# Kernel optimization log

Measured on AMD Instinct MI355X. Metric: run time of the kernel, lower is better.

Reference implementation:

```python
import jax, jax.numpy as jnp
import numpy as np

B, T, D_IN, H, LAT = 256, 512, 32, 128, 64


def lstm_scan(x, Wih, Whh, bih, bhh):
    """PyTorch-convention single-layer LSTM over x [B,T,D] -> hidden states [B,T,H].
    Gate order: i, f, g, o. Gates = x@Wih.T + bih + h@Whh.T + bhh."""
    Bm, _, _ = x.shape
    Hm = Whh.shape[1]
    # precompute input contributions for all timesteps: [B,T,4H]
    xg = jnp.einsum('btd,gd->btg', x, Wih) + bih + bhh

    def step(carry, g_t):
        h, c = carry
        gates = g_t + h @ Whh.T  # [B,4H]
        i, f, g, o = jnp.split(gates, 4, axis=-1)
        i = jax.nn.sigmoid(i)
        f = jax.nn.sigmoid(f)
        g = jnp.tanh(g)
        o = jax.nn.sigmoid(o)
        c = f * c + i * g
        h = o * jnp.tanh(c)
        return (h, c), h

    h0 = jnp.zeros((Bm, Hm), x.dtype)
    (_, _), hs = jax.lax.scan(step, (h0, h0), jnp.swapaxes(xg, 0, 1))
    return jnp.swapaxes(hs, 0, 1)  # [B,T,H]


def setup_inputs() -> dict:
    key = jax.random.key(0)
    ks = jax.random.split(key, 14)
    s = 1.0 / np.sqrt(H)

    def u(k, shape):
        return jax.random.uniform(k, shape, jnp.float32, -s, s)

    return {
        'x': jax.random.normal(ks[0], (B, T, D_IN), jnp.float32),
        # encoder LSTM (input_dim -> hidden)
        'enc_Wih': u(ks[1], (4 * H, D_IN)),
        'enc_Whh': u(ks[2], (4 * H, H)),
        'enc_bih': u(ks[3], (4 * H,)),
        'enc_bhh': u(ks[4], (4 * H,)),
        # encoder linear (hidden -> latent)
        'enc_Wl': u(ks[5], (LAT, H)),
        'enc_bl': u(ks[6], (LAT,)),
        # decoder LSTM (latent -> hidden)
        'dec_Wih': u(ks[7], (4 * H, LAT)),
        'dec_Whh': u(ks[8], (4 * H, H)),
        'dec_bih': u(ks[9], (4 * H,)),
        'dec_bhh': u(ks[10], (4 * H,)),
        # decoder linear (hidden -> input_dim)
        'dec_Wl': u(ks[11], (D_IN, H)),
        'dec_bl': u(ks[12], (D_IN,)),
    }


def reference(x, enc_Wih, enc_Whh, enc_bih, enc_bhh, enc_Wl, enc_bl,
              dec_Wih, dec_Whh, dec_bih, dec_bhh, dec_Wl, dec_bl):
    # Encoder: last hidden state -> linear -> latent
    hs = lstm_scan(x, enc_Wih, enc_Whh, enc_bih, enc_bhh)  # [B,T,H]
    h_last = hs[:, -1]                                     # == hidden.squeeze(0)
    encoded = h_last @ enc_Wl.T + enc_bl                   # [B,LAT]
    # Decoder: repeat latent over time, LSTM, linear
    z = jnp.broadcast_to(encoded[:, None, :], (encoded.shape[0], T, encoded.shape[1]))
    hs2 = lstm_scan(z, dec_Wih, dec_Whh, dec_bih, dec_bhh)  # [B,T,H]
    decoded = hs2 @ dec_Wl.T + dec_bl                       # [B,T,D_IN]
    return encoded, decoded
```

## Files before the change

### kernel.cpp

```cpp
#include <hip/hip_runtime.h>

#define NB   256
#define NT   512
#define NDIN 32
#define NH   128
#define NLAT 64
#define HSTR 136

typedef _Float16 h2 __attribute__((ext_vector_type(2)));
typedef _Float16 h4 __attribute__((ext_vector_type(4)));

__device__ __forceinline__ float dot2(h2 a, h2 b, float c) {
  return __builtin_amdgcn_fdot2(a, b, c, false);
}
__device__ __forceinline__ h2 bc2(float v) { return __builtin_bit_cast(h2, v); }
__device__ __forceinline__ h2 pk2(float a, float b) { return h2{(_Float16)a, (_Float16)b}; }

#define NLOG2E 1.44269504f
__device__ __forceinline__ float sigmoid_f(float x) {
  return __builtin_amdgcn_rcpf(1.f + __builtin_amdgcn_exp2f(x * -NLOG2E));
}
__device__ __forceinline__ float tanh_f(float x) {
  float s = __builtin_amdgcn_rcpf(1.f + __builtin_amdgcn_exp2f(x * (-2.f * NLOG2E)));
  return fmaf(2.f, s, -1.f);
}

template <int CTRL>
__device__ __forceinline__ float dpp_add(float v) {
  int s = __builtin_bit_cast(int, v);
  int p = __builtin_amdgcn_update_dpp(0, s, CTRL, 0xF, 0xF, true);
  return v + __builtin_bit_cast(float, p);
}
__device__ __forceinline__ float quad_reduce(float v) {
  v = dpp_add<0xB1>(v);
  v = dpp_add<0x4E>(v);
  return v;
}

__global__ __launch_bounds__(512, 2) void lstm_ae_kernel(
    const float* __restrict__ x,
    const float* __restrict__ eWih,
    const float* __restrict__ eWhh,
    const float* __restrict__ eBih,
    const float* __restrict__ eBhh,
    const float* __restrict__ eWl,
    const float* __restrict__ eBl,
    const float* __restrict__ dWih,
    const float* __restrict__ dWhh,
    const float* __restrict__ dBih,
    const float* __restrict__ dBhh,
    const float* __restrict__ dWl,
    const float* __restrict__ dBl,
    float* __restrict__ outE,
    float* __restrict__ outD)
{
  extern __shared__ __align__(16) char smem[];
  float*    encs = (float*)smem;
  _Float16* hbuf = (_Float16*)(encs + NLAT);
  _Float16* hist = hbuf + 2 * NH;
  _Float16* xs   = hist;

  const int tid = threadIdx.x;
  const int b   = blockIdx.x;
  const int Q   = tid & 3;
  const int J   = tid >> 2;

  {
    const float4* xg = (const float4*)(x + (size_t)b * (NT * NDIN));
    h4* xo = (h4*)xs;
#pragma unroll
    for (int i = 0; i < 8; ++i) {
      int idx = i * 512 + tid;
      float4 v = xg[idx];
      xo[idx] = h4{(_Float16)v.x, (_Float16)v.y, (_Float16)v.z, (_Float16)v.w};
    }
  }

  h2 wh[4][16];
  h2 wi[4][4];
  float bias[4];
#pragma unroll
  for (int G = 0; G < 4; ++G) {
    const float4* p = (const float4*)(eWhh + (size_t)(G * NH + J) * NH + Q * 32);
#pragma unroll
    for (int f = 0; f < 8; ++f) {
      float4 v = p[f];
      wh[G][2 * f] = pk2(v.x, v.y); wh[G][2 * f + 1] = pk2(v.z, v.w);
    }
    const float4* q = (const float4*)(eWih + (size_t)(G * NH + J) * NDIN + Q * 8);
#pragma unroll
    for (int f = 0; f < 2; ++f) {
      float4 v = q[f];
      wi[G][2 * f] = pk2(v.x, v.y); wi[G][2 * f + 1] = pk2(v.z, v.w);
    }
    bias[G] = eBih[G * NH + J] + eBhh[G * NH + J];
  }
  if (tid < NH) hbuf[tid] = (_Float16)0.f;
  float c = 0.f;
  __syncthreads();

#pragma unroll 1
  for (int t = 0; t < NT; ++t) {
    float a0 = 0.f, a1 = 0.f, a2 = 0.f, a3 = 0.f;
    const float4* hp = (const float4*)(hbuf + (t & 1) * NH + Q * 32);
#pragma unroll
    for (int r = 0; r < 4; ++r) {
      float4 hv = hp[r];
      h2 p0 = bc2(hv.x), p1 = bc2(hv.y), p2 = bc2(hv.z), p3 = bc2(hv.w);
      a0 = dot2(wh[0][4*r+0], p0, a0); a0 = dot2(wh[0][4*r+1], p1, a0);
      a0 = dot2(wh[0][4*r+2], p2, a0); a0 = dot2(wh[0][4*r+3], p3, a0);
      a1 = dot2(wh[1][4*r+0], p0, a1); a1 = dot2(wh[1][4*r+1], p1, a1);
      a1 = dot2(wh[1][4*r+2], p2, a1); a1 = dot2(wh[1][4*r+3], p3, a1);
      a2 = dot2(wh[2][4*r+0], p0, a2); a2 = dot2(wh[2][4*r+1], p1, a2);
      a2 = dot2(wh[2][4*r+2], p2, a2); a2 = dot2(wh[2][4*r+3], p3, a2);
      a3 = dot2(wh[3][4*r+0], p0, a3); a3 = dot2(wh[3][4*r+1], p1, a3);
      a3 = dot2(wh[3][4*r+2], p2, a3); a3 = dot2(wh[3][4*r+3], p3, a3);
    }
    {
      float4 xv = *(const float4*)(xs + t * NDIN + Q * 8);
      h2 p0 = bc2(xv.x), p1 = bc2(xv.y), p2 = bc2(xv.z), p3 = bc2(xv.w);
      a0 = dot2(wi[0][0], p0, a0); a0 = dot2(wi[0][1], p1, a0);
      a0 = dot2(wi[0][2], p2, a0); a0 = dot2(wi[0][3], p3, a0);
      a1 = dot2(wi[1][0], p0, a1); a1 = dot2(wi[1][1], p1, a1);
      a1 = dot2(wi[1][2], p2, a1); a1 = dot2(wi[1][3], p3, a1);
      a2 = dot2(wi[2][0], p0, a2); a2 = dot2(wi[2][1], p1, a2);
      a2 = dot2(wi[2][2], p2, a2); a2 = dot2(wi[2][3], p3, a2);
      a3 = dot2(wi[3][0], p0, a3); a3 = dot2(wi[3][1], p1, a3);
      a3 = dot2(wi[3][2], p2, a3); a3 = dot2(wi[3][3], p3, a3);
    }
    a0 = quad_reduce(a0) + bias[0];
    a1 = quad_reduce(a1) + bias[1];
    a2 = quad_reduce(a2) + bias[2];
    a3 = quad_reduce(a3) + bias[3];
    float gi = sigmoid_f(a0), gf = sigmoid_f(a1);
    float gg = tanh_f(a2),    go = sigmoid_f(a3);
    c = fmaf(gf, c, gi * gg);
    float h = go * tanh_f(c);
    if (Q == 0) hbuf[((t + 1) & 1) * NH + J] = (_Float16)h;
    __syncthreads();
  }

  if (tid < NLAT) {
    const float4* p  = (const float4*)(eWl + (size_t)tid * NH);
    const float2* hh = (const float2*)hbuf;
    float a = eBl[tid];
#pragma unroll
    for (int r = 0; r < 32; ++r) {
      float4 w = p[r];
      float2 hv = hh[r];
      h2 lo = bc2(hv.x), hi = bc2(hv.y);
      a = fmaf((float)lo.x, w.x, a); a = fmaf((float)lo.y, w.y, a);
      a = fmaf((float)hi.x, w.z, a); a = fmaf((float)hi.y, w.w, a);
    }
    encs[tid] = a;
    outE[b * NLAT + tid] = a;
  }
#pragma unroll
  for (int G = 0; G < 4; ++G) {
    const float4* p = (const float4*)(dWhh + (size_t)(G * NH + J) * NH + Q * 32);
#pragma unroll
    for (int f = 0; f < 8; ++f) {
      float4 v = p[f];
      wh[G][2 * f] = pk2(v.x, v.y); wh[G][2 * f + 1] = pk2(v.z, v.w);
    }
  }
  __syncthreads();

  if (tid < NH) hbuf[tid] = (_Float16)0.f;
  c = 0.f;
  float xgd[4];
  {
    const float4* ep = (const float4*)(encs + Q * 16);
    float4 e0 = ep[0], e1 = ep[1], e2 = ep[2], e3 = ep[3];
#pragma unroll
    for (int G = 0; G < 4; ++G) {
      const float4* p = (const float4*)(dWih + (size_t)(G * NH + J) * NLAT + Q * 16);
      float4 w0 = p[0], w1 = p[1], w2 = p[2], w3 = p[3];
      float a;
      a = e0.x * w0.x;        a = fmaf(e0.y, w0.y, a);
      a = fmaf(e0.z, w0.z, a); a = fmaf(e0.w, w0.w, a);
      a = fmaf(e1.x, w1.x, a); a = fmaf(e1.y, w1.y, a);
      a = fmaf(e1.z, w1.z, a); a = fmaf(e1.w, w1.w, a);
      a = fmaf(e2.x, w2.x, a); a = fmaf(e2.y, w2.y, a);
      a = fmaf(e2.z, w2.z, a); a = fmaf(e2.w, w2.w, a);
      a = fmaf(e3.x, w3.x, a); a = fmaf(e3.y, w3.y, a);
      a = fmaf(e3.z, w3.z, a); a = fmaf(e3.w, w3.w, a);
      xgd[G] = quad_reduce(a) + dBih[G * NH + J] + dBhh[G * NH + J];
    }
  }
  __syncthreads();

#pragma unroll 1
  for (int t = 0; t < NT; ++t) {
    float a0 = 0.f, a1 = 0.f, a2 = 0.f, a3 = 0.f;
    const float4* hp = (const float4*)(hbuf + (t & 1) * NH + Q * 32);
#pragma unroll
    for (int r = 0; r < 4; ++r) {
      float4 hv = hp[r];
      h2 p0 = bc2(hv.x), p1 = bc2(hv.y), p2 = bc2(hv.z), p3 = bc2(hv.w);
      a0 = dot2(wh[0][4*r+0], p0, a0); a0 = dot2(wh[0][4*r+1], p1, a0);
      a0 = dot2(wh[0][4*r+2], p2, a0); a0 = dot2(wh[0][4*r+3], p3, a0);
      a1 = dot2(wh[1][4*r+0], p0, a1); a1 = dot2(wh[1][4*r+1], p1, a1);
      a1 = dot2(wh[1][4*r+2], p2, a1); a1 = dot2(wh[1][4*r+3], p3, a1);
      a2 = dot2(wh[2][4*r+0], p0, a2); a2 = dot2(wh[2][4*r+1], p1, a2);
      a2 = dot2(wh[2][4*r+2], p2, a2); a2 = dot2(wh[2][4*r+3], p3, a2);
      a3 = dot2(wh[3][4*r+0], p0, a3); a3 = dot2(wh[3][4*r+1], p1, a3);
      a3 = dot2(wh[3][4*r+2], p2, a3); a3 = dot2(wh[3][4*r+3], p3, a3);
    }
    a0 = quad_reduce(a0) + xgd[0];
    a1 = quad_reduce(a1) + xgd[1];
    a2 = quad_reduce(a2) + xgd[2];
    a3 = quad_reduce(a3) + xgd[3];
    float gi = sigmoid_f(a0), gf = sigmoid_f(a1);
    float gg = tanh_f(a2),    go = sigmoid_f(a3);
    c = fmaf(gf, c, gi * gg);
    float h = go * tanh_f(c);
    if (Q == 0) {
      _Float16 hh = (_Float16)h;
      hbuf[((t + 1) & 1) * NH + J] = hh;
      hist[t * HSTR + J] = hh;
    }
    __syncthreads();
  }

  {
    const int col = tid & 31, rg = tid >> 5;
    h2 wl[64];
    const float4* p0 = (const float4*)(dWl + (size_t)col * NH);
#pragma unroll
    for (int f = 0; f < 32; ++f) {
      float4 v = p0[f];
      wl[2 * f] = pk2(v.x, v.y); wl[2 * f + 1] = pk2(v.z, v.w);
    }
    const float bo = dBl[col];
    float* op = outD + (size_t)b * (NT * NDIN);
#pragma unroll 1
    for (int i = 0; i < 32; ++i) {
      int r = rg + 16 * i;
      const float4* hp = (const float4*)(hist + r * HSTR);
      float s = 0.f;
#pragma unroll
      for (int j = 0; j < 16; ++j) {
        float4 hv = hp[j];
        s = dot2(wl[4*j+0], bc2(hv.x), s);
        s = dot2(wl[4*j+1], bc2(hv.y), s);
        s = dot2(wl[4*j+2], bc2(hv.z), s);
        s = dot2(wl[4*j+3], bc2(hv.w), s);
      }
      op[(size_t)r * NDIN + col] = s + bo;
    }
  }
}

#define SMEM_BYTES (NLAT * 4 + 2 * NH * 2 + NT * HSTR * 2)

extern "C" void kernel_launch(void* const* d_in, const int* in_sizes, int n_in,
                              void* d_out, int out_size, void* d_ws, size_t ws_size,
                              hipStream_t stream) {
  const float* x    = (const float*)d_in[0];
  const float* eWih = (const float*)d_in[1];
  const float* eWhh = (const float*)d_in[2];
  const float* eBih = (const float*)d_in[3];
  const float* eBhh = (const float*)d_in[4];
  const float* eWl  = (const float*)d_in[5];
  const float* eBl  = (const float*)d_in[6];
  const float* dWih = (const float*)d_in[7];
  const float* dWhh = (const float*)d_in[8];
  const float* dBih = (const float*)d_in[9];
  const float* dBhh = (const float*)d_in[10];
  const float* dWl  = (const float*)d_in[11];
  const float* dBl  = (const float*)d_in[12];

  float* outE = (float*)d_out;
  float* outD = outE + (size_t)NB * NLAT;

  (void)hipFuncSetAttribute((const void*)lstm_ae_kernel,
                            hipFuncAttributeMaxDynamicSharedMemorySize,
                            SMEM_BYTES);

  hipLaunchKernelGGL(lstm_ae_kernel, dim3(NB), dim3(512), SMEM_BYTES, stream,
                     x, eWih, eWhh, eBih, eBhh, eWl, eBl,
                     dWih, dWhh, dBih, dBhh, dWl, dBl, outE, outD);
}
```

Measured before the change: 679.3 us.

## Compute LSTM recurrent gate matvec with 16x16x32 f16 MFMA instead of fdot2

Replaces the per-thread fdot2 recurrent and input matvecs with MFMA 16x16x32 f16 instructions. The weight rows are permuted so each lane's accumulator outputs hold the i,f,g,o gates of one hidden unit, which removes the cross-lane quad reduction. Only column 0 of the broadcast h operand is useful, so most MFMA work is wasted. Launch bounds drop to one block per CU, and an extra shared buffer holds the decoder input gates.

```diff
diff --git a/kernel.cpp b/kernel.cpp
--- a/kernel.cpp
+++ b/kernel.cpp
@@ -7,8 +7,10 @@
 #define NLAT 64
 #define HSTR 136
 
-typedef _Float16 h2 __attribute__((ext_vector_type(2)));
-typedef _Float16 h4 __attribute__((ext_vector_type(4)));
+typedef _Float16 f16x8 __attribute__((ext_vector_type(8)));
+typedef float    f32x4 __attribute__((ext_vector_type(4)));
+typedef _Float16 h2    __attribute__((ext_vector_type(2)));
+typedef _Float16 h4    __attribute__((ext_vector_type(4)));
 
 __device__ __forceinline__ float dot2(h2 a, h2 b, float c) {
   return __builtin_amdgcn_fdot2(a, b, c, false);
@@ -24,20 +26,11 @@
   float s = __builtin_amdgcn_rcpf(1.f + __builtin_amdgcn_exp2f(x * (-2.f * NLOG2E)));
   return fmaf(2.f, s, -1.f);
 }
-
-template <int CTRL>
-__device__ __forceinline__ float dpp_add(float v) {
-  int s = __builtin_bit_cast(int, v);
-  int p = __builtin_amdgcn_update_dpp(0, s, CTRL, 0xF, 0xF, true);
-  return v + __builtin_bit_cast(float, p);
-}
-__device__ __forceinline__ float quad_reduce(float v) {
-  v = dpp_add<0xB1>(v);
-  v = dpp_add<0x4E>(v);
-  return v;
-}
-
-__global__ __launch_bounds__(512, 2) void lstm_ae_kernel(
+__device__ __forceinline__ f32x4 mfma16(f16x8 a, f16x8 b, f32x4 c) {
+  return __builtin_amdgcn_mfma_f32_16x16x32_f16(a, b, c, 0, 0, 0);
+}
+
+__global__ __launch_bounds__(512, 1) void lstm_ae_kernel(
     const float* __restrict__ x,
     const float* __restrict__ eWih,
     const float* __restrict__ eWhh,
@@ -56,14 +49,26 @@
 {
   extern __shared__ __align__(16) char smem[];
   float*    encs = (float*)smem;
-  _Float16* hbuf = (_Float16*)(encs + NLAT);
-  _Float16* hist = hbuf + 2 * NH;
+  _Float16* hs   = (_Float16*)(encs + NLAT);
+  _Float16* hist = hs + 2 * NH;
   _Float16* xs   = hist;
+  float*    gtmp = (float*)(hist + NT * HSTR);
 
   const int tid = threadIdx.x;
   const int b   = blockIdx.x;
-  const int Q   = tid & 3;
-  const int J   = tid >> 2;
+  const int w   = tid >> 6;
+  const int l   = tid & 63;
+  const int m   = l & 15;
+  const int kg  = l >> 4;
+  const int ag  = m & 3;
+  const int ar  = 2 * (m >> 2);
+
+  int au[4], cu[4];
+#pragma unroll
+  for (int tt = 0; tt < 4; ++tt) {
+    au[tt] = 16 * w + 8 * (tt >> 1) + ar + (tt & 1);
+    cu[tt] = 16 * w + 8 * (tt >> 1) + 2 * kg + (tt & 1);
+  }
 
   {
     const float4* xg = (const float4*)(x + (size_t)b * (NT * NDIN));
@@ -76,149 +81,141 @@
     }
   }
 
-  h2 wh[4][16];
-  h2 wi[4][4];
-  float bias[4];
-#pragma unroll
-  for (int G = 0; G < 4; ++G) {
-    const float4* p = (const float4*)(eWhh + (size_t)(G * NH + J) * NH + Q * 32);
-#pragma unroll
-    for (int f = 0; f < 8; ++f) {
-      float4 v = p[f];
-      wh[G][2 * f] = pk2(v.x, v.y); wh[G][2 * f + 1] = pk2(v.z, v.w);
-    }
-    const float4* q = (const float4*)(eWih + (size_t)(G * NH + J) * NDIN + Q * 8);
-#pragma unroll
-    for (int f = 0; f < 2; ++f) {
-      float4 v = q[f];
-      wi[G][2 * f] = pk2(v.x, v.y); wi[G][2 * f + 1] = pk2(v.z, v.w);
-    }
-    bias[G] = eBih[G * NH + J] + eBhh[G * NH + J];
-  }
-  if (tid < NH) hbuf[tid] = (_Float16)0.f;
-  float c = 0.f;
+  f16x8 aw[4][4];
+  f16x8 ax[4];
+  f32x4 bi[4];
+#pragma unroll
+  for (int tt = 0; tt < 4; ++tt) {
+    const float* r = eWhh + (size_t)(ag * NH + au[tt]) * NH;
+#pragma unroll
+    for (int K = 0; K < 4; ++K) {
+      const float* p = r + 32 * K + 8 * kg;
+#pragma unroll
+      for (int j = 0; j < 8; ++j) aw[tt][K][j] = (_Float16)p[j];
+    }
+    const float* q = eWih + (size_t)(ag * NH + au[tt]) * NDIN + 8 * kg;
+#pragma unroll
+    for (int j = 0; j < 8; ++j) ax[tt][j] = (_Float16)q[j];
+#pragma unroll
+    for (int j = 0; j < 4; ++j)
+      bi[tt][j] = eBih[j * NH + cu[tt]] + eBhh[j * NH + cu[tt]];
+  }
+  if (tid < 2 * NH) hs[tid] = (_Float16)0.f;
+  float c[4] = {0.f, 0.f, 0.f, 0.f};
   __syncthreads();
 
 #pragma unroll 1
   for (int t = 0; t < NT; ++t) {
-    float a0 = 0.f, a1 = 0.f, a2 = 0.f, a3 = 0.f;
-    const float4* hp = (const float4*)(hbuf + (t & 1) * NH + Q * 32);
-#pragma unroll
-    for (int r = 0; r < 4; ++r) {
-      float4 hv = hp[r];
-      h2 p0 = bc2(hv.x), p1 = bc2(hv.y), p2 = bc2(hv.z), p3 = bc2(hv.w);
-      a0 = dot2(wh[0][4*r+0], p0, a0); a0 = dot2(wh[0][4*r+1], p1, a0);
-      a0 = dot2(wh[0][4*r+2], p2, a0); a0 = dot2(wh[0][4*r+3], p3, a0);
-      a1 = dot2(wh[1][4*r+0], p0, a1); a1 = dot2(wh[1][4*r+1], p1, a1);
-      a1 = dot2(wh[1][4*r+2], p2, a1); a1 = dot2(wh[1][4*r+3], p3, a1);
-      a2 = dot2(wh[2][4*r+0], p0, a2); a2 = dot2(wh[2][4*r+1], p1, a2);
-      a2 = dot2(wh[2][4*r+2], p2, a2); a2 = dot2(wh[2][4*r+3], p3, a2);
-      a3 = dot2(wh[3][4*r+0], p0, a3); a3 = dot2(wh[3][4*r+1], p1, a3);
-      a3 = dot2(wh[3][4*r+2], p2, a3); a3 = dot2(wh[3][4*r+3], p3, a3);
+    f32x4 acc[4];
+#pragma unroll
+    for (int tt = 0; tt < 4; ++tt) acc[tt] = bi[tt];
+    const _Float16* hb = hs + (t & 1) * NH;
+#pragma unroll
+    for (int K = 0; K < 4; ++K) {
+      f16x8 bf = *(const f16x8*)(hb + 32 * K + 8 * kg);
+#pragma unroll
+      for (int tt = 0; tt < 4; ++tt) acc[tt] = mfma16(aw[tt][K], bf, acc[tt]);
     }
     {
-      float4 xv = *(const float4*)(xs + t * NDIN + Q * 8);
-      h2 p0 = bc2(xv.x), p1 = bc2(xv.y), p2 = bc2(xv.z), p3 = bc2(xv.w);
-      a0 = dot2(wi[0][0], p0, a0); a0 = dot2(wi[0][1], p1, a0);
-      a0 = dot2(wi[0][2], p2, a0); a0 = dot2(wi[0][3], p3, a0);
-      a1 = dot2(wi[1][0], p0, a1); a1 = dot2(wi[1][1], p1, a1);
-      a1 = dot2(wi[1][2], p2, a1); a1 = dot2(wi[1][3], p3, a1);
-      a2 = dot2(wi[2][0], p0, a2); a2 = dot2(wi[2][1], p1, a2);
-      a2 = dot2(wi[2][2], p2, a2); a2 = dot2(wi[2][3], p3, a2);
-      a3 = dot2(wi[3][0], p0, a3); a3 = dot2(wi[3][1], p1, a3);
-      a3 = dot2(wi[3][2], p2, a3); a3 = dot2(wi[3][3], p3, a3);
-    }
-    a0 = quad_reduce(a0) + bias[0];
-    a1 = quad_reduce(a1) + bias[1];
-    a2 = quad_reduce(a2) + bias[2];
-    a3 = quad_reduce(a3) + bias[3];
-    float gi = sigmoid_f(a0), gf = sigmoid_f(a1);
-    float gg = tanh_f(a2),    go = sigmoid_f(a3);
-    c = fmaf(gf, c, gi * gg);
-    float h = go * tanh_f(c);
-    if (Q == 0) hbuf[((t + 1) & 1) * NH + J] = (_Float16)h;
+      f16x8 xf = *(const f16x8*)(xs + t * NDIN + 8 * kg);
+#pragma unroll
+      for (int tt = 0; tt < 4; ++tt) acc[tt] = mfma16(ax[tt], xf, acc[tt]);
+    }
+    float hv[4];
+#pragma unroll
+    for (int tt = 0; tt < 4; ++tt) {
+      float gi = sigmoid_f(acc[tt][0]);
+      float gf = sigmoid_f(acc[tt][1]);
+      float gg = tanh_f(acc[tt][2]);
+      float go = sigmoid_f(acc[tt][3]);
+      c[tt] = fmaf(gf, c[tt], gi * gg);
+      hv[tt] = go * tanh_f(c[tt]);
+    }
+    if (m == 0) {
+      _Float16* hn = hs + ((t + 1) & 1) * NH;
+      *(h2*)(hn + cu[0]) = pk2(hv[0], hv[1]);
+      *(h2*)(hn + cu[2]) = pk2(hv[2], hv[3]);
+    }
     __syncthreads();
   }
 
   if (tid < NLAT) {
     const float4* p  = (const float4*)(eWl + (size_t)tid * NH);
-    const float2* hh = (const float2*)hbuf;
+    const float2* hh = (const float2*)hs;
     float a = eBl[tid];
 #pragma unroll
     for (int r = 0; r < 32; ++r) {
-      float4 w = p[r];
-      float2 hv = hh[r];
-      h2 lo = bc2(hv.x), hi = bc2(hv.y);
-      a = fmaf((float)lo.x, w.x, a); a = fmaf((float)lo.y, w.y, a);
-      a = fmaf((float)hi.x, w.z, a); a = fmaf((float)hi.y, w.w, a);
+      float4 wv = p[r];
+      float2 hp = hh[r];
+      h2 lov = bc2(hp.x), hiv = bc2(hp.y);
+      a = fmaf((float)lov.x, wv.x, a); a = fmaf((float)lov.y, wv.y, a);
+      a = fmaf((float)hiv.x, wv.z, a); a = fmaf((float)hiv.y, wv.w, a);
     }
     encs[tid] = a;
     outE[b * NLAT + tid] = a;
   }
 #pragma unroll
-  for (int G = 0; G < 4; ++G) {
-    const float4* p = (const float4*)(dWhh + (size_t)(G * NH + J) * NH + Q * 32);
-#pragma unroll
-    for (int f = 0; f < 8; ++f) {
-      float4 v = p[f];
-      wh[G][2 * f] = pk2(v.x, v.y); wh[G][2 * f + 1] = pk2(v.z, v.w);
+  for (int tt = 0; tt < 4; ++tt) {
+    const float* r = dWhh + (size_t)(ag * NH + au[tt]) * NH;
+#pragma unroll
+    for (int K = 0; K < 4; ++K) {
+      const float* p = r + 32 * K + 8 * kg;
+#pragma unroll
+      for (int j = 0; j < 8; ++j) aw[tt][K][j] = (_Float16)p[j];
     }
   }
   __syncthreads();
 
-  if (tid < NH) hbuf[tid] = (_Float16)0.f;
-  c = 0.f;
-  float xgd[4];
+  if (tid < 2 * NH) hs[tid] = (_Float16)0.f;
   {
-    const float4* ep = (const float4*)(encs + Q * 16);
-    float4 e0 = ep[0], e1 = ep[1], e2 = ep[2], e3 = ep[3];
-#pragma unroll
-    for (int G = 0; G < 4; ++G) {
-      const float4* p = (const float4*)(dWih + (size_t)(G * NH + J) * NLAT + Q * 16);
-      float4 w0 = p[0], w1 = p[1], w2 = p[2], w3 = p[3];
-      float a;
-      a = e0.x * w0.x;        a = fmaf(e0.y, w0.y, a);
-      a = fmaf(e0.z, w0.z, a); a = fmaf(e0.w, w0.w, a);
-      a = fmaf(e1.x, w1.x, a); a = fmaf(e1.y, w1.y, a);
-      a = fmaf(e1.z, w1.z, a); a = fmaf(e1.w, w1.w, a);
-      a = fmaf(e2.x, w2.x, a); a = fmaf(e2.y, w2.y, a);
-      a = fmaf(e2.z, w2.z, a); a = fmaf(e2.w, w2.w, a);
-      a = fmaf(e3.x, w3.x, a); a = fmaf(e3.y, w3.y, a);
-      a = fmaf(e3.z, w3.z, a); a = fmaf(e3.w, w3.w, a);
-      xgd[G] = quad_reduce(a) + dBih[G * NH + J] + dBhh[G * NH + J];
-    }
+    const float4* p  = (const float4*)(dWih + (size_t)tid * NLAT);
+    const float4* e4 = (const float4*)encs;
+    float a = dBih[tid] + dBhh[tid];
+#pragma unroll
+    for (int r = 0; r < 16; ++r) {
+      float4 wv = p[r]; float4 ev = e4[r];
+      a = fmaf(ev.x, wv.x, a); a = fmaf(ev.y, wv.y, a);
+      a = fmaf(ev.z, wv.z, a); a = fmaf(ev.w, wv.w, a);
+    }
+    gtmp[tid] = a;
   }
   __syncthreads();
+#pragma unroll
+  for (int tt = 0; tt < 4; ++tt) {
+#pragma unroll
+    for (int j = 0; j < 4; ++j) bi[tt][j] = gtmp[j * NH + cu[tt]];
+    c[tt] = 0.f;
+  }
 
 #pragma unroll 1
   for (int t = 0; t < NT; ++t) {
-    float a0 = 0.f, a1 = 0.f, a2 = 0.f, a3 = 0.f;
-    const float4* hp = (const float4*)(hbuf + (t & 1) * NH + Q * 32);
-#pragma unroll
-    for (int r = 0; r < 4; ++r) {
-      float4 hv = hp[r];
-      h2 p0 = bc2(hv.x), p1 = bc2(hv.y), p2 = bc2(hv.z), p3 = bc2(hv.w);
-      a0 = dot2(wh[0][4*r+0], p0, a0); a0 = dot2(wh[0][4*r+1], p1, a0);
-      a0 = dot2(wh[0][4*r+2], p2, a0); a0 = dot2(wh[0][4*r+3], p3, a0);
-      a1 = dot2(wh[1][4*r+0], p0, a1); a1 = dot2(wh[1][4*r+1], p1, a1);
-      a1 = dot2(wh[1][4*r+2], p2, a1); a1 = dot2(wh[1][4*r+3], p3, a1);
-      a2 = dot2(wh[2][4*r+0], p0, a2); a2 = dot2(wh[2][4*r+1], p1, a2);
-      a2 = dot2(wh[2][4*r+2], p2, a2); a2 = dot2(wh[2][4*r+3], p3, a2);
-      a3 = dot2(wh[3][4*r+0], p0, a3); a3 = dot2(wh[3][4*r+1], p1, a3);
-      a3 = dot2(wh[3][4*r+2], p2, a3); a3 = dot2(wh[3][4*r+3], p3, a3);
-    }
-    a0 = quad_reduce(a0) + xgd[0];
-    a1 = quad_reduce(a1) + xgd[1];
-    a2 = quad_reduce(a2) + xgd[2];
-    a3 = quad_reduce(a3) + xgd[3];
-    float gi = sigmoid_f(a0), gf = sigmoid_f(a1);
-    float gg = tanh_f(a2),    go = sigmoid_f(a3);
-    c = fmaf(gf, c, gi * gg);
-    float h = go * tanh_f(c);
-    if (Q == 0) {
-      _Float16 hh = (_Float16)h;
-      hbuf[((t + 1) & 1) * NH + J] = hh;
-      hist[t * HSTR + J] = hh;
+    f32x4 acc[4];
+#pragma unroll
+    for (int tt = 0; tt < 4; ++tt) acc[tt] = bi[tt];
+    const _Float16* hb = hs + (t & 1) * NH;
+#pragma unroll
+    for (int K = 0; K < 4; ++K) {
+      f16x8 bf = *(const f16x8*)(hb + 32 * K + 8 * kg);
+#pragma unroll
+      for (int tt = 0; tt < 4; ++tt) acc[tt] = mfma16(aw[tt][K], bf, acc[tt]);
+    }
+    float hv[4];
+#pragma unroll
+    for (int tt = 0; tt < 4; ++tt) {
+      float gi = sigmoid_f(acc[tt][0]);
+      float gf = sigmoid_f(acc[tt][1]);
+      float gg = tanh_f(acc[tt][2]);
+      float go = sigmoid_f(acc[tt][3]);
+      c[tt] = fmaf(gf, c[tt], gi * gg);
+      hv[tt] = go * tanh_f(c[tt]);
+    }
+    if (m == 0) {
+      _Float16* hn = hs + ((t + 1) & 1) * NH;
+      *(h2*)(hn + cu[0]) = pk2(hv[0], hv[1]);
+      *(h2*)(hn + cu[2]) = pk2(hv[2], hv[3]);
+      _Float16* hr = hist + t * HSTR;
+      *(h2*)(hr + cu[0]) = pk2(hv[0], hv[1]);
+      *(h2*)(hr + cu[2]) = pk2(hv[2], hv[3]);
     }
     __syncthreads();
   }
@@ -241,18 +238,18 @@
       float s = 0.f;
 #pragma unroll
       for (int j = 0; j < 16; ++j) {
-        float4 hv = hp[j];
-        s = dot2(wl[4*j+0], bc2(hv.x), s);
-        s = dot2(wl[4*j+1], bc2(hv.y), s);
-        s = dot2(wl[4*j+2], bc2(hv.z), s);
-        s = dot2(wl[4*j+3], bc2(hv.w), s);
+        float4 hvv = hp[j];
+        s = dot2(wl[4 * j + 0], bc2(hvv.x), s);
+        s = dot2(wl[4 * j + 1], bc2(hvv.y), s);
+        s = dot2(wl[4 * j + 2], bc2(hvv.z), s);
+        s = dot2(wl[4 * j + 3], bc2(hvv.w), s);
       }
       op[(size_t)r * NDIN + col] = s + bo;
     }
   }
 }
 
-#define SMEM_BYTES (NLAT * 4 + 2 * NH * 2 + NT * HSTR * 2)
+#define SMEM_BYTES (NLAT * 4 + 2 * NH * 2 + NT * HSTR * 2 + 512 * 4)
 
 extern "C" void kernel_launch(void* const* d_in, const int* in_sizes, int n_in,
                               void* d_out, int out_size, void* d_ws, size_t ws_size,
```

Result: slower. 887.0 us (+30.6%).
